# Kernel optimization log

Measured on AMD Instinct MI355X. Metric: run time of the kernel, lower is better.

## Reference

```python
import jax, jax.numpy as jnp
import numpy as np

L = 8          # fixed number of instance labels (0 = background), all assumed present
DV = 0.5       # delta_v
DD = 1.5       # delta_d
LOSS_WEIGHT = 1.0


def _safe_norm(x, axis):
    sq = jnp.sum(x * x, axis=axis)
    pos = sq > 0
    return jnp.sqrt(jnp.where(pos, sq, 1.0)) * pos.astype(x.dtype)


def _per_image(emb, inst, kern, tmask):
    # emb: [D,H,W], inst: [H,W] int, kern/tmask: [H,W] float
    D, H, W = emb.shape
    HW = H * W
    tm = (tmask > 0.5).astype(inst.dtype)
    kb = (kern > 0.5).astype(inst.dtype)
    inst = inst * tm
    inst_k = (inst * kb).reshape(-1)          # kernel-region labels
    inst_f = inst.reshape(-1)                 # full-region labels
    emb_f = emb.reshape(D, -1).T              # [HW, D]

    # --- generate_coef: first/second occurrence (row-major) of each label ---
    flat = jnp.arange(HW)
    eq = inst_f[None, :] == jnp.arange(L)[:, None]          # [L, HW]
    idxs = jnp.where(eq, flat[None, :], HW)
    first = jnp.min(idxs, axis=1)
    second = jnp.min(jnp.where(idxs == first[:, None], HW, idxs), axis=1)
    first = jnp.minimum(first, HW - 1)
    second = jnp.minimum(second, HW - 1)
    r0, c0 = first // W, first % W
    r1, c1 = second // W, second % W
    # pos_id = (tmp[0,0], tmp[1,0], tmp[0,-1], tmp[1,-1]) as in the source
    pos = jnp.stack([r0, r1, c0, c1], axis=1).astype(jnp.float32)  # [L,4]
    diag = jnp.sqrt(jnp.float32(H * H + W * W))
    coef_diag = jnp.exp(jnp.sqrt((pos[:, 0] - pos[:, 2]) ** 2 +
                                 (pos[:, 1] - pos[:, 3]) ** 2) / diag / 2.0)
    zmask = (jnp.arange(L) > 0).astype(jnp.float32)          # skip label 0
    coef_diag = coef_diag * zmask
    s = pos[:, 0] + pos[:, 2]
    t = pos[:, 1] + pos[:, 3]
    dp = jnp.sqrt((s[:, None] - s[None, :]) ** 2 + (t[:, None] - t[None, :]) ** 2)
    coef_off = 1.0 - 20.0 * jnp.exp(-4.0 - 2.5 * dp / diag)
    eye = jnp.eye(L, dtype=bool)
    coef = jnp.where(eye, coef_diag[:, None], coef_off)
    coef = coef * zmask[:, None] * zmask[None, :]

    # --- per-label kernel means (segment mean) ---
    ones = jnp.ones((HW,), jnp.float32)
    cnt_k = jax.ops.segment_sum(ones, inst_k, num_segments=L)
    mean = jax.ops.segment_sum(emb_f, inst_k, num_segments=L)
    mean = mean / jnp.maximum(cnt_k, 1.0)[:, None]           # [L, D]
    mean = mean * zmask[:, None]

    # --- l_agg: per-pixel distance to own-label mean, segment-mean per label ---
    mean_px = mean[inst_f]                                   # [HW, D] gather
    dist = _safe_norm(emb_f - mean_px, axis=1)
    cd_px = coef_diag[inst_f]
    val = jnp.log(jax.nn.relu(cd_px * dist - DV) ** 2 + 1.0)
    cnt = jax.ops.segment_sum(ones, inst_f, num_segments=L)
    l_agg_per = jax.ops.segment_sum(val, inst_f, num_segments=L) / jnp.maximum(cnt, 1.0)
    l_agg = jnp.mean(l_agg_per[1:])

    # --- l_dis: coefficient-weighted pairwise hinge between means ---
    Dn = _safe_norm(mean[:, None, :] - mean[None, :, :], axis=-1)  # [L, L]
    pm = (~eye) & (zmask[:, None] > 0) & (zmask[None, :] > 0)
    vals = jnp.log(jax.nn.relu(2.0 * DD - coef * Dn) ** 2 + 1.0)
    l_dis = jnp.sum(jnp.where(pm, vals, 0.0)) / ((L - 1) * (L - 2))

    # --- l_reg ---
    l_reg = jnp.mean(jnp.log(_safe_norm(mean, axis=1) + 1.0)) * 0.001
    return l_agg + l_dis + l_reg


def reference(emb, instance, kernel, training_mask, bboxes):
    # bboxes is accepted but unused, matching the original forward_single
    loss_batch = jax.vmap(_per_image)(emb, instance, kernel, training_mask)
    return LOSS_WEIGHT * jnp.mean(loss_batch)


def setup_inputs() -> dict:
    key = jax.random.key(0)
    k1, k2, k3, k4, k5 = jax.random.split(key, 5)
    B, D, H, W = 8, 4, 640, 640
    emb = jax.random.normal(k1, (B, D, H, W), dtype=jnp.float32)
    instance = jax.random.randint(k2, (B, H, W), 0, L, dtype=jnp.int32)
    kernel = jax.random.uniform(k3, (B, H, W), dtype=jnp.float32)
    training_mask = jax.random.uniform(k4, (B, H, W), dtype=jnp.float32)
    bboxes = jax.random.uniform(k5, (B, 10, 4), dtype=jnp.float32)
    return {"emb": emb, "instance": instance, "kernel": kernel,
            "training_mask": training_mask, "bboxes": bboxes}
```

## Files before the change

kernel.cpp:

```cpp
#include <hip/hip_runtime.h>
#include <hip/hip_bf16.h>

#define B_    8
#define D_    4
#define H_    640
#define W_    640
#define HW_   (H_ * W_)
#define L_    8
#define NL    (L_ - 1)
#define BLOCK 256
#define VITER 4
#define GRIDX (HW_ / (BLOCK * 4 * VITER))

__device__ __forceinline__ void gatom_add(float* p, float v) {
    unsafeAtomicAdd(p, v);
}

__global__ void k_init(int* ib) {
    int t = threadIdx.x;
    if (t < 128) ib[t] = HW_;
    ib[128 + t] = 0;
    if (t < 136) ib[384 + t] = 0;
}

__global__ __launch_bounds__(BLOCK, 2) void k_pass1(
        const float* __restrict__ emb, const int* __restrict__ inst,
        const float* __restrict__ kern, const float* __restrict__ tmask,
        int* __restrict__ firstIdx, int* __restrict__ secondIdx,
        int* __restrict__ cntf_i, int* __restrict__ cntk_i,
        float* __restrict__ sumemb) {
    __shared__ int   sCnt[L_];
    __shared__ float sSum[L_ * D_];
    __shared__ int   sM1[L_], sM2[L_];

    const int tid = threadIdx.x;
    if (tid < L_) { sCnt[tid] = 0; sM1[tid] = HW_; sM2[tid] = HW_; }
    if (tid < L_ * D_) sSum[tid] = 0.f;
    __syncthreads();

    const int b = blockIdx.y;
    const int blockbase = blockIdx.x * (BLOCK * 4 * VITER);
    const float* embb = emb + (size_t)b * D_ * HW_;
    const int base = b * HW_;

    int   cnt[NL];
    float sm[NL][D_];
    int   m1[NL], m2[NL];
    #pragma unroll
    for (int l = 0; l < NL; ++l) {
        cnt[l] = 0; m1[l] = HW_; m2[l] = HW_;
        #pragma unroll
        for (int d = 0; d < D_; ++d) sm[l][d] = 0.f;
    }

    #pragma unroll
    for (int it = 0; it < VITER; ++it) {
        const int off = blockbase + it * (BLOCK * 4) + tid * 4;
        const int4   lab4 = *(const int4*)  (inst  + base + off);
        const float4 tm4  = *(const float4*)(tmask + base + off);
        const float4 kn4  = *(const float4*)(kern  + base + off);
        const float4 ev0  = *(const float4*)(embb + 0 * HW_ + off);
        const float4 ev1  = *(const float4*)(embb + 1 * HW_ + off);
        const float4 ev2  = *(const float4*)(embb + 2 * HW_ + off);
        const float4 ev3  = *(const float4*)(embb + 3 * HW_ + off);
        const int   labA[4] = {lab4.x, lab4.y, lab4.z, lab4.w};
        const float tmA[4]  = {tm4.x, tm4.y, tm4.z, tm4.w};
        const float knA[4]  = {kn4.x, kn4.y, kn4.z, kn4.w};
        const float e0A[4]  = {ev0.x, ev0.y, ev0.z, ev0.w};
        const float e1A[4]  = {ev1.x, ev1.y, ev1.z, ev1.w};
        const float e2A[4]  = {ev2.x, ev2.y, ev2.z, ev2.w};
        const float e3A[4]  = {ev3.x, ev3.y, ev3.z, ev3.w};

        #pragma unroll
        for (int c = 0; c < 4; ++c) {
            const int p  = off + c;
            const int lf = (tmA[c] > 0.5f) ? labA[c] : 0;
            const bool kb = (knA[c] > 0.5f);
            #pragma unroll
            for (int l = 1; l < L_; ++l) {
                const int k = l - 1;
                const bool pf = (lf == l);
                const bool pk = pf && kb;
                cnt[k] += (pf ? 0x10000 : 0) + (pk ? 1 : 0);
                const float mk = pk ? 1.0f : 0.0f;
                sm[k][0] += mk * e0A[c];
                sm[k][1] += mk * e1A[c];
                sm[k][2] += mk * e2A[c];
                sm[k][3] += mk * e3A[c];
                const bool t1 = pf && (m1[k] == HW_);
                const bool t2 = pf && !t1 && (m2[k] == HW_);
                m1[k] = t1 ? p : m1[k];
                m2[k] = t2 ? p : m2[k];
            }
        }
    }

    #pragma unroll
    for (int l = 0; l < NL; ++l) {
        #pragma unroll
        for (int off = 32; off > 0; off >>= 1) {
            cnt[l]   += __shfl_down(cnt[l], off);
            sm[l][0] += __shfl_down(sm[l][0], off);
            sm[l][1] += __shfl_down(sm[l][1], off);
            sm[l][2] += __shfl_down(sm[l][2], off);
            sm[l][3] += __shfl_down(sm[l][3], off);
            int o1 = __shfl_down(m1[l], off);
            int o2 = __shfl_down(m2[l], off);
            m2[l] = min(min(m2[l], o2), max(m1[l], o1));
            m1[l] = min(m1[l], o1);
        }
    }

    if ((tid & 63) == 0) {
        #pragma unroll
        for (int l = 0; l < NL; ++l) {
            atomicAdd(&sCnt[l + 1], cnt[l]);
            #pragma unroll
            for (int d = 0; d < D_; ++d) atomicAdd(&sSum[(l + 1) * D_ + d], sm[l][d]);
            int old = atomicMin(&sM1[l + 1], m1[l]);
            atomicMin(&sM2[l + 1], max(old, m1[l]));
            atomicMin(&sM2[l + 1], m2[l]);
        }
    }
    __syncthreads();

    if (tid >= 1 && tid < L_) {
        atomicAdd(&cntf_i[b * L_ + tid], sCnt[tid] >> 16);
        atomicAdd(&cntk_i[b * L_ + tid], sCnt[tid] & 0xFFFF);
        int old = atomicMin(&firstIdx[b * L_ + tid], sM1[tid]);
        atomicMin(&secondIdx[b * L_ + tid], max(old, sM1[tid]));
        atomicMin(&secondIdx[b * L_ + tid], sM2[tid]);
    }
    if (tid >= D_ && tid < L_ * D_)
        gatom_add(&sumemb[b * L_ * D_ + tid], sSum[tid]);
}

__global__ __launch_bounds__(BLOCK, 2) void k_pass3(
        const float* __restrict__ emb, const int* __restrict__ inst,
        const float* __restrict__ tmask,
        const int* __restrict__ firstIdx, const int* __restrict__ secondIdx,
        const int* __restrict__ cntk_i, const int* __restrict__ cntf_i,
        const float* __restrict__ sumemb, float* __restrict__ sumvalb) {
    __shared__ float4 sMean[L_];
    __shared__ float  sCd[L_], sInv[L_];
    __shared__ float  sAcc;

    const int tid = threadIdx.x;
    const int b   = blockIdx.y;

    if (tid < L_) {
        float4 mu = {0.f, 0.f, 0.f, 0.f};
        float cd = 0.f, inv = 0.f;
        if (tid > 0) {
            const float invk = 1.0f / fmaxf((float)cntk_i[b * L_ + tid], 1.0f);
            mu.x = sumemb[b * L_ * D_ + tid * D_ + 0] * invk;
            mu.y = sumemb[b * L_ * D_ + tid * D_ + 1] * invk;
            mu.z = sumemb[b * L_ * D_ + tid * D_ + 2] * invk;
            mu.w = sumemb[b * L_ * D_ + tid * D_ + 3] * invk;
            const float diag = sqrtf((float)(H_ * H_ + W_ * W_));
            int f = min(firstIdx[b * L_ + tid],  HW_ - 1);
            int s = min(secondIdx[b * L_ + tid], HW_ - 1);
            float r0 = (float)(f / W_), c0 = (float)(f % W_);
            float r1 = (float)(s / W_), c1 = (float)(s % W_);
            cd = __expf(sqrtf((r0 - c0) * (r0 - c0) + (r1 - c1) * (r1 - c1))
                        / diag * 0.5f);
            inv = 1.0f / fmaxf((float)cntf_i[b * L_ + tid], 1.0f);
        }
        sMean[tid] = mu; sCd[tid] = cd; sInv[tid] = inv;
        if (tid == 0) sAcc = 0.f;
    }
    __syncthreads();

    const int blockbase = blockIdx.x * (BLOCK * 4 * VITER);
    const float* embb = emb + (size_t)b * D_ * HW_;
    const int base = b * HW_;
    float acc = 0.f;

    #pragma unroll
    for (int it = 0; it < VITER; ++it) {
        const int off = blockbase + it * (BLOCK * 4) + tid * 4;
        const int4   lab4 = *(const int4*)  (inst  + base + off);
        const float4 tm4  = *(const float4*)(tmask + base + off);
        const float4 ev0  = *(const float4*)(embb + 0 * HW_ + off);
        const float4 ev1  = *(const float4*)(embb + 1 * HW_ + off);
        const float4 ev2  = *(const float4*)(embb + 2 * HW_ + off);
        const float4 ev3  = *(const float4*)(embb + 3 * HW_ + off);
        const int   labA[4] = {lab4.x, lab4.y, lab4.z, lab4.w};
        const float tmA[4]  = {tm4.x, tm4.y, tm4.z, tm4.w};
        const float e0A[4]  = {ev0.x, ev0.y, ev0.z, ev0.w};
        const float e1A[4]  = {ev1.x, ev1.y, ev1.z, ev1.w};
        const float e2A[4]  = {ev2.x, ev2.y, ev2.z, ev2.w};
        const float e3A[4]  = {ev3.x, ev3.y, ev3.z, ev3.w};

        #pragma unroll
        for (int c = 0; c < 4; ++c) {
            const int lf = (tmA[c] > 0.5f) ? labA[c] : 0;
            const float4 mu = sMean[lf];
            float dx = e0A[c] - mu.x, dy = e1A[c] - mu.y;
            float dz = e2A[c] - mu.z, dw = e3A[c] - mu.w;
            float d2 = dx * dx + dy * dy + dz * dz + dw * dw;
            float x  = fmaxf(sCd[lf] * sqrtf(d2) - 0.5f, 0.0f);
            acc += __logf(x * x + 1.0f) * sInv[lf];
        }
    }

    #pragma unroll
    for (int off = 32; off > 0; off >>= 1)
        acc += __shfl_down(acc, off);
    if ((tid & 63) == 0) atomicAdd(&sAcc, acc);
    __syncthreads();
    if (tid == 0) gatom_add(&sumvalb[b], sAcc);
}

__global__ __launch_bounds__(512) void k_final(
        const int* __restrict__ firstIdx, const int* __restrict__ secondIdx,
        const int* __restrict__ cntk_i, const float* __restrict__ sumemb,
        const float* __restrict__ sumvalb, float* __restrict__ out) {
    __shared__ float sWave[8];
    const int tid = threadIdx.x;
    const int b = tid >> 6, ij = tid & 63, i = ij >> 3, j = ij & 7;
    const float diag = sqrtf((float)(H_ * H_ + W_ * W_));

    float mi[D_], mj[D_];
    {
        float ci = 1.0f / fmaxf((float)cntk_i[b * L_ + i], 1.0f);
        float cj = 1.0f / fmaxf((float)cntk_i[b * L_ + j], 1.0f);
        #pragma unroll
        for (int d = 0; d < D_; ++d) {
            mi[d] = (i > 0) ? sumemb[(b * L_ + i) * D_ + d] * ci : 0.0f;
            mj[d] = (j > 0) ? sumemb[(b * L_ + j) * D_ + d] * cj : 0.0f;
        }
    }

    float contrib = 0.0f;
    if (j == 0) {
        float d2 = 0.f;
        #pragma unroll
        for (int d = 0; d < D_; ++d) d2 += mi[d] * mi[d];
        float n = (d2 > 0.f) ? sqrtf(d2) : 0.f;
        contrib += __logf(n + 1.0f) * (0.001f / (float)L_);
    }
    if (i == 0 && j == 1)
        contrib += sumvalb[b] * (1.0f / (float)NL);
    if (i >= 1 && j >= 1 && i != j) {
        float d2 = 0.f;
        #pragma unroll
        for (int d = 0; d < D_; ++d) {
            float df = mi[d] - mj[d];
            d2 += df * df;
        }
        float Dn = (d2 > 0.f) ? sqrtf(d2) : 0.f;
        int fi = min(firstIdx[b * L_ + i],  HW_ - 1);
        int si = min(secondIdx[b * L_ + i], HW_ - 1);
        int fj = min(firstIdx[b * L_ + j],  HW_ - 1);
        int sj = min(secondIdx[b * L_ + j], HW_ - 1);
        float ssi = (float)(fi / W_) + (float)(fi % W_);
        float tti = (float)(si / W_) + (float)(si % W_);
        float ssj = (float)(fj / W_) + (float)(fj % W_);
        float ttj = (float)(sj / W_) + (float)(sj % W_);
        float dx = ssi - ssj, dy = tti - ttj;
        float dp = sqrtf(dx * dx + dy * dy);
        float coef = 1.0f - 20.0f * __expf(-4.0f - 2.5f * dp / diag);
        float x = fmaxf(3.0f - coef * Dn, 0.0f);
        contrib += __logf(x * x + 1.0f) * (1.0f / 42.0f);
    }

    #pragma unroll
    for (int off = 32; off > 0; off >>= 1)
        contrib += __shfl_down(contrib, off);
    if ((tid & 63) == 0) sWave[tid >> 6] = contrib;
    __syncthreads();
    if (tid == 0) {
        float t = 0.f;
        #pragma unroll
        for (int w = 0; w < 8; ++w) t += sWave[w];
        out[0] = t * (1.0f / (float)B_);
    }
}

extern "C" void kernel_launch(void* const* d_in, const int* in_sizes, int n_in,
                              void* d_out, int out_size, void* d_ws, size_t ws_size,
                              hipStream_t stream) {
    const float* emb   = (const float*)d_in[0];
    const int*   inst  = (const int*)  d_in[1];
    const float* kern  = (const float*)d_in[2];
    const float* tmask = (const float*)d_in[3];

    int*   ib        = (int*)d_ws;
    int*   firstIdx  = ib;
    int*   secondIdx = ib + 64;
    int*   cntf_i    = ib + 128;
    int*   cntk_i    = ib + 192;
    float* sumemb    = (float*)(ib + 256);
    float* sumvalb   = (float*)(ib + 512);
    float* out       = (float*)d_out;

    dim3 grid(GRIDX, B_);

    k_init <<<1, 256, 0, stream>>>(ib);
    k_pass1<<<grid, BLOCK, 0, stream>>>(emb, inst, kern, tmask,
                                        firstIdx, secondIdx, cntf_i, cntk_i, sumemb);
    k_pass3<<<grid, BLOCK, 0, stream>>>(emb, inst, tmask, firstIdx, secondIdx,
                                        cntk_i, cntf_i, sumemb, sumvalb);
    k_final<<<1, 512, 0, stream>>>(firstIdx, secondIdx, cntk_i,
                                   sumemb, sumvalb, out);
}
```

Before: 159.5 us.

## Use wave ballots for label counts and LDS atomics for per-label sums

```diff
diff --git a/kernel.cpp b/kernel.cpp
--- a/kernel.cpp
+++ b/kernel.cpp
@@ -9,7 +9,7 @@
 #define L_    8
 #define NL    (L_ - 1)
 #define BLOCK 256
-#define VITER 4
+#define VITER 2
 #define GRIDX (HW_ / (BLOCK * 4 * VITER))
 
 __device__ __forceinline__ void gatom_add(float* p, float v) {
@@ -23,19 +23,20 @@
     if (t < 136) ib[384 + t] = 0;
 }
 
-__global__ __launch_bounds__(BLOCK, 2) void k_pass1(
+__global__ __launch_bounds__(BLOCK, 4) void k_pass1(
         const float* __restrict__ emb, const int* __restrict__ inst,
         const float* __restrict__ kern, const float* __restrict__ tmask,
         int* __restrict__ firstIdx, int* __restrict__ secondIdx,
         int* __restrict__ cntf_i, int* __restrict__ cntk_i,
         float* __restrict__ sumemb) {
+    __shared__ float sSum[D_][NL][64];
     __shared__ int   sCnt[L_];
-    __shared__ float sSum[L_ * D_];
     __shared__ int   sM1[L_], sM2[L_];
 
-    const int tid = threadIdx.x;
+    const int tid  = threadIdx.x;
+    const int lane = tid & 63;
     if (tid < L_) { sCnt[tid] = 0; sM1[tid] = HW_; sM2[tid] = HW_; }
-    if (tid < L_ * D_) sSum[tid] = 0.f;
+    for (int i = tid; i < D_ * NL * 64; i += BLOCK) ((float*)sSum)[i] = 0.f;
     __syncthreads();
 
     const int b = blockIdx.y;
@@ -43,19 +44,14 @@
     const float* embb = emb + (size_t)b * D_ * HW_;
     const int base = b * HW_;
 
-    int   cnt[NL];
-    float sm[NL][D_];
-    int   m1[NL], m2[NL];
-    #pragma unroll
-    for (int l = 0; l < NL; ++l) {
-        cnt[l] = 0; m1[l] = HW_; m2[l] = HW_;
-        #pragma unroll
-        for (int d = 0; d < D_; ++d) sm[l][d] = 0.f;
-    }
+    int cf[NL], ck[NL], m1[NL], m2[NL];
+    #pragma unroll
+    for (int l = 0; l < NL; ++l) { cf[l] = 0; ck[l] = 0; m1[l] = HW_; m2[l] = HW_; }
 
     #pragma unroll
     for (int it = 0; it < VITER; ++it) {
         const int off = blockbase + it * (BLOCK * 4) + tid * 4;
+        const int Sbase = blockbase + it * (BLOCK * 4) + (tid & ~63) * 4;
         const int4   lab4 = *(const int4*)  (inst  + base + off);
         const float4 tm4  = *(const float4*)(tmask + base + off);
         const float4 kn4  = *(const float4*)(kern  + base + off);
@@ -71,52 +67,46 @@
         const float e2A[4]  = {ev2.x, ev2.y, ev2.z, ev2.w};
         const float e3A[4]  = {ev3.x, ev3.y, ev3.z, ev3.w};
 
+        bool done[NL];
+        #pragma unroll
+        for (int l = 0; l < NL; ++l) done[l] = (m2[l] != HW_);
+
         #pragma unroll
         for (int c = 0; c < 4; ++c) {
-            const int p  = off + c;
             const int lf = (tmA[c] > 0.5f) ? labA[c] : 0;
             const bool kb = (knA[c] > 0.5f);
+            const unsigned long long kbm = __ballot(kb);
             #pragma unroll
             for (int l = 1; l < L_; ++l) {
                 const int k = l - 1;
-                const bool pf = (lf == l);
-                const bool pk = pf && kb;
-                cnt[k] += (pf ? 0x10000 : 0) + (pk ? 1 : 0);
-                const float mk = pk ? 1.0f : 0.0f;
-                sm[k][0] += mk * e0A[c];
-                sm[k][1] += mk * e1A[c];
-                sm[k][2] += mk * e2A[c];
-                sm[k][3] += mk * e3A[c];
-                const bool t1 = pf && (m1[k] == HW_);
-                const bool t2 = pf && !t1 && (m2[k] == HW_);
-                m1[k] = t1 ? p : m1[k];
-                m2[k] = t2 ? p : m2[k];
+                const unsigned long long m = __ballot(lf == l);
+                cf[k] += __popcll(m);
+                ck[k] += __popcll(m & kbm);
+                if (!done[k] && m != 0ULL) {
+                    const int S  = Sbase + c;
+                    const int a1 = S + 4 * (int)__builtin_ctzll(m);
+                    const unsigned long long mm = m & (m - 1);
+                    const int a2 = mm ? S + 4 * (int)__builtin_ctzll(mm) : HW_;
+                    const int lo = min(m1[k], a1);
+                    const int hi = max(m1[k], a1);
+                    m1[k] = lo;
+                    m2[k] = min(min(m2[k], a2), hi);
+                }
             }
-        }
-    }
-
-    #pragma unroll
-    for (int l = 0; l < NL; ++l) {
-        #pragma unroll
-        for (int off = 32; off > 0; off >>= 1) {
-            cnt[l]   += __shfl_down(cnt[l], off);
-            sm[l][0] += __shfl_down(sm[l][0], off);
-            sm[l][1] += __shfl_down(sm[l][1], off);
-            sm[l][2] += __shfl_down(sm[l][2], off);
-            sm[l][3] += __shfl_down(sm[l][3], off);
-            int o1 = __shfl_down(m1[l], off);
-            int o2 = __shfl_down(m2[l], off);
-            m2[l] = min(min(m2[l], o2), max(m1[l], o1));
-            m1[l] = min(m1[l], o1);
-        }
-    }
-
-    if ((tid & 63) == 0) {
+            if (lf > 0 && kb) {
+                const int li = lf - 1;
+                atomicAdd(&sSum[0][li][lane], e0A[c]);
+                atomicAdd(&sSum[1][li][lane], e1A[c]);
+                atomicAdd(&sSum[2][li][lane], e2A[c]);
+                atomicAdd(&sSum[3][li][lane], e3A[c]);
+            }
+        }
+    }
+
+    if (lane == 0) {
         #pragma unroll
         for (int l = 0; l < NL; ++l) {
-            atomicAdd(&sCnt[l + 1], cnt[l]);
-            #pragma unroll
-            for (int d = 0; d < D_; ++d) atomicAdd(&sSum[(l + 1) * D_ + d], sm[l][d]);
+            atomicAdd(&sCnt[l + 1], (cf[l] << 16) | ck[l]);
             int old = atomicMin(&sM1[l + 1], m1[l]);
             atomicMin(&sM2[l + 1], max(old, m1[l]));
             atomicMin(&sM2[l + 1], m2[l]);
@@ -124,18 +114,34 @@
     }
     __syncthreads();
 
+    {
+        const int w = tid >> 6;
+        float v[NL];
+        #pragma unroll
+        for (int l = 0; l < NL; ++l) v[l] = sSum[w][l][lane];
+        #pragma unroll
+        for (int off = 32; off > 0; off >>= 1) {
+            #pragma unroll
+            for (int l = 0; l < NL; ++l) v[l] += __shfl_down(v[l], off);
+        }
+        if (lane == 0) {
+            #pragma unroll
+            for (int l = 0; l < NL; ++l)
+                gatom_add(&sumemb[(b * L_ + l + 1) * D_ + w], v[l]);
+        }
+    }
+
     if (tid >= 1 && tid < L_) {
-        atomicAdd(&cntf_i[b * L_ + tid], sCnt[tid] >> 16);
-        atomicAdd(&cntk_i[b * L_ + tid], sCnt[tid] & 0xFFFF);
+        const int pc = sCnt[tid];
+        atomicAdd(&cntf_i[b * L_ + tid], pc >> 16);
+        atomicAdd(&cntk_i[b * L_ + tid], pc & 0xFFFF);
         int old = atomicMin(&firstIdx[b * L_ + tid], sM1[tid]);
         atomicMin(&secondIdx[b * L_ + tid], max(old, sM1[tid]));
         atomicMin(&secondIdx[b * L_ + tid], sM2[tid]);
     }
-    if (tid >= D_ && tid < L_ * D_)
-        gatom_add(&sumemb[b * L_ * D_ + tid], sSum[tid]);
-}
-
-__global__ __launch_bounds__(BLOCK, 2) void k_pass3(
+}
+
+__global__ __launch_bounds__(BLOCK, 4) void k_pass3(
         const float* __restrict__ emb, const int* __restrict__ inst,
         const float* __restrict__ tmask,
         const int* __restrict__ firstIdx, const int* __restrict__ secondIdx,
```

New measurement: 236.6 us. 48.3% more time.
